# Performance work log

Hardware: AMD Instinct MI355X
Metric: run time of the kernel (lower is better)

The kernel has to match this reference:

```python
import jax, jax.numpy as jnp
import numpy as np

A = 2
IMG_C = 3
IMG_H = 64
IMG_W = 96
N_OBJ = 5   # OBJS + STACKS with REMOVE_BG
B = 64
P = 4       # number of predicate nets
CONV_OUT = 32


def setup_inputs() -> dict:
    key = jax.random.key(0)
    k0, k1, k2, k3 = jax.random.split(key, 4)
    state = jax.random.normal(k0, (B, N_OBJ, IMG_C, IMG_H, IMG_W), jnp.float32)
    state_next = jax.random.normal(k1, (B, N_OBJ, IMG_C, IMG_H, IMG_W), jnp.float32)
    # uniform object count (structural max N=5) so tuple count is static
    n_obj = jnp.full((B,), N_OBJ, dtype=jnp.int32)
    temp = jnp.float32(0.5)
    # stacked params for the P predicate nets (conv + linear head)
    conv_w = jax.random.normal(k2, (P * CONV_OUT, A * IMG_C, 3, 3), jnp.float32) * 0.05
    conv_b = jnp.zeros((P * CONV_OUT,), jnp.float32)
    w2 = jax.random.normal(k3, (P, CONV_OUT), jnp.float32) * 0.1
    b2 = jnp.zeros((P,), jnp.float32)
    return {"state": state, "state_next": state_next, "conv_w": conv_w,
            "conv_b": conv_b, "w2": w2, "b2": b2, "n_obj": n_obj, "temp": temp}


def _build_tuples(s, n):
    # cartesian_prod(arange(n), arange(n)) -> ordered pairs (i, j)
    ii = jnp.repeat(jnp.arange(n), n)   # [n*n]
    jj = jnp.tile(jnp.arange(n), n)     # [n*n]
    a = s[:, ii]                        # [B, n*n, C, H, W]
    b = s[:, jj]
    t = jnp.concatenate([a, b], axis=2)             # [B, n*n, A*C, H, W]
    return t.reshape(-1, A * IMG_C, IMG_H, IMG_W)   # [B*n*n, 6, H, W]


def _predicates(t, conv_w, conv_b, w2, b2, temp):
    # fused conv over all P nets (stacked output channels)
    y = jax.lax.conv_general_dilated(
        t, conv_w, window_strides=(2, 2), padding='SAME',
        dimension_numbers=('NCHW', 'OIHW', 'NCHW'))
    y = jax.nn.relu(y + conv_b[None, :, None, None])
    y = y.mean(axis=(2, 3)).reshape(-1, P, CONV_OUT)   # [T, P, 32]
    logits = jnp.einsum('tpc,pc->tp', y, w2) + b2      # [T, P]
    return jax.nn.sigmoid(logits / temp)


def reference(state, state_next, conv_w, conv_b, w2, b2, n_obj, temp):
    n = N_OBJ  # uniform ragged case: all n_obj entries equal the max
    tuples = _build_tuples(state, n)
    tuples_next = _build_tuples(state_next, n)
    preds = _predicates(tuples, conv_w, conv_b, w2, b2, temp)
    preds_next = _predicates(tuples_next, conv_w, conv_b, w2, b2, temp)
    # adjacency: column per tuple, one-hot in the owning sample's row
    T = B * n * n
    adj = (jnp.arange(T)[None, :] // (n * n) == jnp.arange(B)[:, None]).astype(jnp.float32)
    return preds, preds_next, adj
```

## Files before the change

kernel.cpp:

```cpp
#include <hip/hip_runtime.h>
#include <math.h>

#define BQ 64
#define NOBJ 5
#define CIN 3
#define IMG_H 64
#define IMG_W 96
#define OH 32
#define OW 48
#define NPAIR 25
#define PP 4
#define CONV_OUT 32

#define NRG 16
#define NPOS 96
#define XK 32
#define X_U32 (NOBJ * NPOS * XK / 2)
#define X_UNITS (NOBJ * NPOS * 4)

#define NPRED (2 * 1600 * PP)
#define ADJ_N (BQ * 1600)

typedef __fp16   h2 __attribute__((ext_vector_type(2)));
typedef _Float16 half8 __attribute__((ext_vector_type(8)));
typedef float    float4_ __attribute__((ext_vector_type(4)));
typedef unsigned int uint4_ __attribute__((ext_vector_type(4)));

__global__ __launch_bounds__(512) void conv_pair_mfma(
    const float* __restrict__ state,
    const float* __restrict__ state_next,
    const float* __restrict__ conv_w,
    const float* __restrict__ conv_b,
    const float* __restrict__ w2,
    float* __restrict__ T,
    float* __restrict__ out)
{
    __shared__ __align__(16) unsigned int sX32[X_U32];

    const int tid = threadIdx.x;
    const int rg  = blockIdx.x;
    const int b   = blockIdx.y;
    const int src = blockIdx.z;

    const float* g = (src == 0 ? state : state_next)
                   + (size_t)b * NOBJ * CIN * IMG_H * IMG_W;
    const int R0 = rg * 4;

    if (src == 1 && tid < 100) {
        int a  = (rg + NRG * b) * 100 + tid;
        int bb = a / 1600;
        int t  = a - bb * 1600;
        out[NPRED + a] = (t / NPAIR == bb) ? 1.0f : 0.0f;
    }

    const int wave = tid >> 6;
    const int lane = tid & 63;
    const int quad = lane >> 4;
    const int ocl  = lane & 15;

    const int mt  = wave;
    const int p   = mt >> 1;
    const int row = mt * 16 + ocl;

    half8 wa, wb;
    #pragma unroll
    for (int j = 0; j < 8; ++j) {
        int k = quad * 8 + j;
        float va = 0.f, vb = 0.f;
        if (k < 27) {
            va = conv_w[row * 54 + k];
            vb = conv_w[row * 54 + 27 + k];
        } else if (k == 27) {
            va = conv_b[row];
        }
        wa[j] = (_Float16)va;
        wb[j] = (_Float16)vb;
    }
    h2 w2h01, w2h23;
    {
        const float* wp = w2 + p * CONV_OUT + (mt & 1) * 16 + quad * 4;
        w2h01 = __builtin_amdgcn_cvt_pkrtz(wp[0], wp[1]);
        w2h23 = __builtin_amdgcn_cvt_pkrtz(wp[2], wp[3]);
    }

    {
        const int subk = tid & 3;
        int koff[8], khv[8], kwv[8];
        float padf[8];
        bool kval[8];
        #pragma unroll
        for (int j = 0; j < 8; ++j) {
            int k = subk * 8 + j;
            if (k < 27) {
                int ci = k / 9;
                int r9 = k - ci * 9;
                int kh = r9 / 3;
                int kw = r9 - kh * 3;
                koff[j] = ci * (IMG_H * IMG_W) + kh * IMG_W + kw;
                khv[j] = kh; kwv[j] = kw; kval[j] = true; padf[j] = 0.f;
            } else {
                koff[j] = 0; khv[j] = 0; kwv[j] = 0; kval[j] = false;
                padf[j] = (k == 27) ? 1.0f : 0.f;
            }
        }
        for (int u = tid; u < X_UNITS; u += 512) {
            int pl  = (u >> 2) % NPOS;
            int obj = u / (NPOS * 4);
            int rl  = (pl >= 48) ? 1 : 0;
            int pc  = pl - rl * 48;
            int gr0 = R0 + 2 * rl;
            int gc0 = 2 * pc;
            const float* gp = g + obj * (CIN * IMG_H * IMG_W) + gr0 * IMG_W + gc0;
            float fv[8];
            #pragma unroll
            for (int j = 0; j < 8; ++j) {
                float v = padf[j];
                if (kval[j] && (gr0 + khv[j] < IMG_H) && (gc0 + kwv[j] < IMG_W))
                    v = gp[koff[j]];
                fv[j] = v;
            }
            uint4_ w4;
            w4.x = __builtin_bit_cast(unsigned int, __builtin_amdgcn_cvt_pkrtz(fv[0], fv[1]));
            w4.y = __builtin_bit_cast(unsigned int, __builtin_amdgcn_cvt_pkrtz(fv[2], fv[3]));
            w4.z = __builtin_bit_cast(unsigned int, __builtin_amdgcn_cvt_pkrtz(fv[4], fv[5]));
            w4.w = __builtin_bit_cast(unsigned int, __builtin_amdgcn_cvt_pkrtz(fv[6], fv[7]));
            *(uint4_*)&sX32[(size_t)u * 4] = w4;
        }
    }

    __syncthreads();

    const float4_ zero4 = {0.f, 0.f, 0.f, 0.f};
    const h2 hz = {(__fp16)0.f, (__fp16)0.f};

    float acc[NPAIR];
    #pragma unroll
    for (int q = 0; q < NPAIR; ++q) acc[q] = 0.f;

    #pragma unroll
    for (int nt = 0; nt < 6; ++nt) {
        const int rl  = nt / 3;
        const int c0  = (nt - rl * 3) * 16;
        const int pos = rl * 48 + c0 + ocl;

        half8 xf[NOBJ];
        h2 ah01[NOBJ], ah23[NOBJ];
        #pragma unroll
        for (int obj = 0; obj < NOBJ; ++obj) {
            xf[obj] = *(const half8*)&sX32[((size_t)(obj * NPOS + pos)) * 16 + quad * 4];
            float4_ a = __builtin_amdgcn_mfma_f32_16x16x32_f16(wa, xf[obj], zero4, 0, 0, 0);
            ah01[obj] = __builtin_amdgcn_cvt_pkrtz(a[0], a[1]);
            ah23[obj] = __builtin_amdgcn_cvt_pkrtz(a[2], a[3]);
        }

        #pragma unroll
        for (int jo = 0; jo < NOBJ; ++jo) {
            float4_ bq = __builtin_amdgcn_mfma_f32_16x16x32_f16(wb, xf[jo], zero4, 0, 0, 0);
            h2 bh01 = __builtin_amdgcn_cvt_pkrtz(bq[0], bq[1]);
            h2 bh23 = __builtin_amdgcn_cvt_pkrtz(bq[2], bq[3]);
            #pragma unroll
            for (int i = 0; i < NOBJ; ++i) {
                h2 s0 = ah01[i] + bh01;
                h2 s1 = ah23[i] + bh23;
                s0 = __builtin_elementwise_max(s0, hz);
                s1 = __builtin_elementwise_max(s1, hz);
                float t0 = __builtin_amdgcn_fdot2(s0, w2h01, acc[i * NOBJ + jo], false);
                acc[i * NOBJ + jo] = __builtin_amdgcn_fdot2(s1, w2h23, t0, false);
            }
        }
    }

    float myv = 0.f;
    #pragma unroll
    for (int q = 0; q < NPAIR; ++q) {
        float rr = acc[q];
        #pragma unroll
        for (int off = 32; off > 0; off >>= 1)
            rr += __shfl_xor(rr, off, 64);
        if (lane == q) myv = rr;
    }
    if (lane < NPAIR)
        T[((((size_t)src * BQ + b) * NRG + rg) * NPAIR + lane) * 8 + mt] = myv;
}

__global__ __launch_bounds__(256) void pred_kernel(
    const float* __restrict__ T,
    const float* __restrict__ b2,
    const float* __restrict__ temp,
    float* __restrict__ out)
{
    int idx = blockIdx.x * blockDim.x + threadIdx.x;
    if (idx >= NPRED) return;
    int p   = idx & 3;
    int t   = (idx >> 2) % 1600;
    int src = idx / 6400;
    int bb  = t / NPAIR;
    int pr  = t - bb * NPAIR;
    const float* base = T + ((((size_t)src * BQ + bb) * NRG) * NPAIR + pr) * 8 + 2 * p;
    float sum = 0.f;
    #pragma unroll
    for (int rgi = 0; rgi < NRG; ++rgi) {
        sum += base[(size_t)rgi * NPAIR * 8];
        sum += base[(size_t)rgi * NPAIR * 8 + 1];
    }
    float logit = sum * (1.0f / (OH * OW)) + b2[p];
    float x = logit / temp[0];
    out[idx] = 1.0f / (1.0f + expf(-x));
}

extern "C" void kernel_launch(void* const* d_in, const int* in_sizes, int n_in,
                              void* d_out, int out_size, void* d_ws, size_t ws_size,
                              hipStream_t stream)
{
    const float* state      = (const float*)d_in[0];
    const float* state_next = (const float*)d_in[1];
    const float* conv_w     = (const float*)d_in[2];
    const float* conv_b     = (const float*)d_in[3];
    const float* w2         = (const float*)d_in[4];
    const float* b2         = (const float*)d_in[5];
    const float* temp       = (const float*)d_in[7];

    float* out = (float*)d_out;
    float* T   = (float*)d_ws;

    dim3 grid1(NRG, BQ, 2);
    conv_pair_mfma<<<grid1, 512, 0, stream>>>(state, state_next, conv_w, conv_b,
                                              w2, T, out);

    pred_kernel<<<(NPRED + 255) / 256, 256, 0, stream>>>(T, b2, temp, out);
}
```

Measured before the change: 152.5 us.

## Use MFMA for w2 head dot, swizzle LDS, split pair passes, parallelize pred reduce

Replaces the per-pair fdot2 head reduction with 16x16x16 MFMA accumulation into float4 accumulators, processed in two passes over the i-objects to limit register pressure. It adds an XOR swizzle on the LDS layout to reduce bank conflicts, sets launch_bounds occupancy to 4, and moves the final cross-lane reduction to fewer shuffles. The pred kernel uses four threads per output with vector loads and shuffle reduction. The MFMA trick performs redundant work because only the diagonal or sum is needed, and the two passes repeat the LDS loads and the wb MFMAs.

```diff
diff --git a/kernel.cpp b/kernel.cpp
--- a/kernel.cpp
+++ b/kernel.cpp
@@ -22,11 +22,15 @@
 #define ADJ_N (BQ * 1600)
 
 typedef __fp16   h2 __attribute__((ext_vector_type(2)));
+typedef _Float16 half4_t __attribute__((ext_vector_type(4)));
 typedef _Float16 half8 __attribute__((ext_vector_type(8)));
 typedef float    float4_ __attribute__((ext_vector_type(4)));
+typedef float    float2_ __attribute__((ext_vector_type(2)));
 typedef unsigned int uint4_ __attribute__((ext_vector_type(4)));
 
-__global__ __launch_bounds__(512) void conv_pair_mfma(
+struct h2x2 { h2 lo, hi; };
+
+__global__ __launch_bounds__(512, 4) void conv_pair_mfma(
     const float* __restrict__ state,
     const float* __restrict__ state_next,
     const float* __restrict__ conv_w,
@@ -76,11 +80,13 @@
         wa[j] = (_Float16)va;
         wb[j] = (_Float16)vb;
     }
-    h2 w2h01, w2h23;
+    half4_t w2f;
     {
         const float* wp = w2 + p * CONV_OUT + (mt & 1) * 16 + quad * 4;
-        w2h01 = __builtin_amdgcn_cvt_pkrtz(wp[0], wp[1]);
-        w2h23 = __builtin_amdgcn_cvt_pkrtz(wp[2], wp[3]);
+        h2x2 pk;
+        pk.lo = __builtin_amdgcn_cvt_pkrtz(wp[0], wp[1]);
+        pk.hi = __builtin_amdgcn_cvt_pkrtz(wp[2], wp[3]);
+        w2f = __builtin_bit_cast(half4_t, pk);
     }
 
     {
@@ -124,7 +130,8 @@
             w4.y = __builtin_bit_cast(unsigned int, __builtin_amdgcn_cvt_pkrtz(fv[2], fv[3]));
             w4.z = __builtin_bit_cast(unsigned int, __builtin_amdgcn_cvt_pkrtz(fv[4], fv[5]));
             w4.w = __builtin_bit_cast(unsigned int, __builtin_amdgcn_cvt_pkrtz(fv[6], fv[7]));
-            *(uint4_*)&sX32[(size_t)u * 4] = w4;
+            int swk = subk ^ ((pl >> 1) & 3);
+            *(uint4_*)&sX32[(size_t)(obj * (NPOS * 16) + pl * 16 + swk * 4)] = w4;
         }
     }
 
@@ -133,54 +140,70 @@
     const float4_ zero4 = {0.f, 0.f, 0.f, 0.f};
     const h2 hz = {(__fp16)0.f, (__fp16)0.f};
 
-    float acc[NPAIR];
+    float pairval = 0.f;
+
     #pragma unroll
-    for (int q = 0; q < NPAIR; ++q) acc[q] = 0.f;
-
-    #pragma unroll
-    for (int nt = 0; nt < 6; ++nt) {
-        const int rl  = nt / 3;
-        const int c0  = (nt - rl * 3) * 16;
-        const int pos = rl * 48 + c0 + ocl;
-
-        half8 xf[NOBJ];
-        h2 ah01[NOBJ], ah23[NOBJ];
-        #pragma unroll
-        for (int obj = 0; obj < NOBJ; ++obj) {
-            xf[obj] = *(const half8*)&sX32[((size_t)(obj * NPOS + pos)) * 16 + quad * 4];
-            float4_ a = __builtin_amdgcn_mfma_f32_16x16x32_f16(wa, xf[obj], zero4, 0, 0, 0);
-            ah01[obj] = __builtin_amdgcn_cvt_pkrtz(a[0], a[1]);
-            ah23[obj] = __builtin_amdgcn_cvt_pkrtz(a[2], a[3]);
-        }
-
-        #pragma unroll
-        for (int jo = 0; jo < NOBJ; ++jo) {
-            float4_ bq = __builtin_amdgcn_mfma_f32_16x16x32_f16(wb, xf[jo], zero4, 0, 0, 0);
-            h2 bh01 = __builtin_amdgcn_cvt_pkrtz(bq[0], bq[1]);
-            h2 bh23 = __builtin_amdgcn_cvt_pkrtz(bq[2], bq[3]);
-            #pragma unroll
-            for (int i = 0; i < NOBJ; ++i) {
-                h2 s0 = ah01[i] + bh01;
-                h2 s1 = ah23[i] + bh23;
-                s0 = __builtin_elementwise_max(s0, hz);
-                s1 = __builtin_elementwise_max(s1, hz);
-                float t0 = __builtin_amdgcn_fdot2(s0, w2h01, acc[i * NOBJ + jo], false);
-                acc[i * NOBJ + jo] = __builtin_amdgcn_fdot2(s1, w2h23, t0, false);
-            }
-        }
-    }
-
-    float myv = 0.f;
-    #pragma unroll
-    for (int q = 0; q < NPAIR; ++q) {
-        float rr = acc[q];
-        #pragma unroll
-        for (int off = 32; off > 0; off >>= 1)
-            rr += __shfl_xor(rr, off, 64);
-        if (lane == q) myv = rr;
-    }
+    for (int pass = 0; pass < 2; ++pass) {
+        const int I0 = pass ? 3 : 0;
+        const int NI = pass ? 2 : 3;
+
+        float4_ acc2[3 * NOBJ];
+        #pragma unroll
+        for (int q = 0; q < 3 * NOBJ; ++q) acc2[q] = zero4;
+
+        #pragma unroll
+        for (int nt = 0; nt < 6; ++nt) {
+            const int rl  = nt / 3;
+            const int c0  = (nt - rl * 3) * 16;
+            const int pos = rl * 48 + c0 + ocl;
+            const int sw  = (pos >> 1) & 3;
+            const int sbase = pos * 16 + ((quad ^ sw) << 2);
+
+            half8 xf[NOBJ];
+            #pragma unroll
+            for (int obj = 0; obj < NOBJ; ++obj)
+                xf[obj] = *(const half8*)&sX32[sbase + obj * (NPOS * 16)];
+
+            h2 ah01[3], ah23[3];
+            #pragma unroll
+            for (int ii = 0; ii < NI; ++ii) {
+                float4_ a = __builtin_amdgcn_mfma_f32_16x16x32_f16(wa, xf[I0 + ii], zero4, 0, 0, 0);
+                ah01[ii] = __builtin_amdgcn_cvt_pkrtz(a[0], a[1]);
+                ah23[ii] = __builtin_amdgcn_cvt_pkrtz(a[2], a[3]);
+            }
+
+            #pragma unroll
+            for (int jo = 0; jo < NOBJ; ++jo) {
+                float4_ bqv = __builtin_amdgcn_mfma_f32_16x16x32_f16(wb, xf[jo], zero4, 0, 0, 0);
+                h2 bh01 = __builtin_amdgcn_cvt_pkrtz(bqv[0], bqv[1]);
+                h2 bh23 = __builtin_amdgcn_cvt_pkrtz(bqv[2], bqv[3]);
+                #pragma unroll
+                for (int ii = 0; ii < NI; ++ii) {
+                    h2 s0 = __builtin_elementwise_max(ah01[ii] + bh01, hz);
+                    h2 s1 = __builtin_elementwise_max(ah23[ii] + bh23, hz);
+                    h2x2 pk; pk.lo = s0; pk.hi = s1;
+                    half4_t a2 = __builtin_bit_cast(half4_t, pk);
+                    acc2[ii * NOBJ + jo] =
+                        __builtin_amdgcn_mfma_f32_16x16x16f16(a2, w2f, acc2[ii * NOBJ + jo], 0, 0, 0);
+                }
+            }
+        }
+
+        #pragma unroll
+        for (int ii = 0; ii < NI; ++ii) {
+            #pragma unroll
+            for (int jo = 0; jo < NOBJ; ++jo) {
+                float4_ d = acc2[ii * NOBJ + jo];
+                float r = (d[0] + d[1]) + (d[2] + d[3]);
+                r += __shfl_xor(r, 16, 64);
+                r += __shfl_xor(r, 32, 64);
+                if (lane == (I0 + ii) * NOBJ + jo) pairval = r;
+            }
+        }
+    }
+
     if (lane < NPAIR)
-        T[((((size_t)src * BQ + b) * NRG + rg) * NPAIR + lane) * 8 + mt] = myv;
+        T[((((size_t)src * BQ + b) * NRG + rg) * NPAIR + lane) * 8 + mt] = pairval;
 }
 
 __global__ __launch_bounds__(256) void pred_kernel(
@@ -189,7 +212,9 @@
     const float* __restrict__ temp,
     float* __restrict__ out)
 {
-    int idx = blockIdx.x * blockDim.x + threadIdx.x;
+    int gid = blockIdx.x * blockDim.x + threadIdx.x;
+    int idx = gid >> 2;
+    int h   = gid & 3;
     if (idx >= NPRED) return;
     int p   = idx & 3;
     int t   = (idx >> 2) % 1600;
@@ -199,13 +224,18 @@
     const float* base = T + ((((size_t)src * BQ + bb) * NRG) * NPAIR + pr) * 8 + 2 * p;
     float sum = 0.f;
     #pragma unroll
-    for (int rgi = 0; rgi < NRG; ++rgi) {
-        sum += base[(size_t)rgi * NPAIR * 8];
-        sum += base[(size_t)rgi * NPAIR * 8 + 1];
-    }
-    float logit = sum * (1.0f / (OH * OW)) + b2[p];
-    float x = logit / temp[0];
-    out[idx] = 1.0f / (1.0f + expf(-x));
+    for (int r = 0; r < 4; ++r) {
+        int rgi = h * 4 + r;
+        float2_ v = *(const float2_*)&base[(size_t)rgi * NPAIR * 8];
+        sum += v[0] + v[1];
+    }
+    sum += __shfl_xor(sum, 1, 64);
+    sum += __shfl_xor(sum, 2, 64);
+    if (h == 0) {
+        float logit = sum * (1.0f / (OH * OW)) + b2[p];
+        float x = logit / temp[0];
+        out[idx] = 1.0f / (1.0f + expf(-x));
+    }
 }
 
 extern "C" void kernel_launch(void* const* d_in, const int* in_sizes, int n_in,
@@ -227,5 +257,5 @@
     conv_pair_mfma<<<grid1, 512, 0, stream>>>(state, state_next, conv_w, conv_b,
                                               w2, T, out);
 
-    pred_kernel<<<(NPRED + 255) / 256, 256, 0, stream>>>(T, b2, temp, out);
+    pred_kernel<<<(NPRED * 4 + 255) / 256, 256, 0, stream>>>(T, b2, temp, out);
 }
```

Measured after the change: 275.9 us. +80.9%, slower.
